# Kernel optimization log

Measured on AMD Instinct MI355X. Metric: run time of the kernel, lower is better.

Reference implementation:

```python
import jax, jax.numpy as jnp
import numpy as np

EMBED = 1024
HEADS = 16
HEAD_DIM = EMBED // HEADS


def setup_inputs() -> dict:
    key = jax.random.key(0)
    ks = jax.random.split(key, 8)
    N, S = 4, 2048
    inp = {
        "values": jax.random.normal(ks[0], (N, S, EMBED), jnp.float32),
        "keys": jax.random.normal(ks[1], (N, S, EMBED), jnp.float32),
        "queries": jax.random.normal(ks[2], (N, S, EMBED), jnp.float32),
        "mask": jnp.ones((N, S), jnp.int32),  # unused by the original forward
        # learned params (torch Linear: y = x @ W.T + b)
        "Wv": jax.random.normal(ks[3], (HEAD_DIM, HEAD_DIM), jnp.float32) / np.sqrt(HEAD_DIM),
        "Wk": jax.random.normal(ks[4], (HEAD_DIM, HEAD_DIM), jnp.float32) / np.sqrt(HEAD_DIM),
        "Wq": jax.random.normal(ks[5], (HEAD_DIM, HEAD_DIM), jnp.float32) / np.sqrt(HEAD_DIM),
        "Wo": jax.random.normal(ks[6], (EMBED, EMBED), jnp.float32) / np.sqrt(EMBED),
        "bo": jax.random.normal(ks[7], (EMBED,), jnp.float32) * 0.01,
    }
    return inp


def reference(values, keys, queries, mask, Wv, Wk, Wq, Wo, bo):
    N, S, _ = queries.shape
    # reshape to (N, len, heads, head_dim)
    v = values.reshape(N, S, HEADS, HEAD_DIM)
    k = keys.reshape(N, S, HEADS, HEAD_DIM)
    q = queries.reshape(N, S, HEADS, HEAD_DIM)
    # per-head linear projections (weights shared across heads), y = x @ W.T
    v = jnp.einsum('nlhd,ed->nlhe', v, Wv)
    k = jnp.einsum('nlhd,ed->nlhe', k, Wk)
    q = jnp.einsum('nlhd,ed->nlhe', q, Wq)
    # attention scores scaled by sqrt(embed_size), faithful to original
    scores = jnp.einsum('nqhd,nkhd->nhqk', q, k) / jnp.sqrt(jnp.float32(EMBED))
    attn = jax.nn.softmax(scores, axis=3)
    out = jnp.einsum('nhql,nlhd->nqhd', attn, v).reshape(N, S, EMBED)
    return out @ Wo.T + bo
```

## Files before the change

kernel.cpp:

```cpp
#include <hip/hip_runtime.h>


using f32x4  = __attribute__((ext_vector_type(4))) float;
using f32x16 = __attribute__((ext_vector_type(16))) float;
using bf16x8 = __attribute__((ext_vector_type(8))) __bf16;
using u32x4  = __attribute__((ext_vector_type(4))) unsigned int;
using u16x8  = __attribute__((ext_vector_type(8))) unsigned short;
typedef unsigned short u16;
typedef unsigned int   u32;
typedef unsigned long long u64;

#define SEQ 2048
#define EMB 1024
#define NHEADS 16
#define HDIM 64
#define NBATCH 4
#define NH 64

__device__ __forceinline__ u16 f2bf(float f) {
  u32 u = __builtin_bit_cast(u32, f);
  return (u16)((u + 0x7fffu + ((u >> 16) & 1u)) >> 16);
}

__device__ __forceinline__ u32 cvtpk_bf16(float a, float b) {
  u32 d;
  asm("v_cvt_pk_bf16_f32 %0, %1, %2" : "=v"(d) : "v"(a), "v"(b));
  return d;
}

__device__ __forceinline__ f32x4 mfma16(bf16x8 a, bf16x8 b, f32x4 c) {
  return __builtin_amdgcn_mfma_f32_16x16x32_bf16(a, b, c, 0, 0, 0);
}

__device__ __forceinline__ f32x16 mfma32(bf16x8 a, bf16x8 b, f32x16 c) {
  return __builtin_amdgcn_mfma_f32_32x32x16_bf16(a, b, c, 0, 0, 0);
}

__device__ __forceinline__ bf16x8 cvt8(f32x4 a, f32x4 b) {
  u32x4 r;
  r[0] = cvtpk_bf16(a[0], a[1]);
  r[1] = cvtpk_bf16(a[2], a[3]);
  r[2] = cvtpk_bf16(b[0], b[1]);
  r[3] = cvtpk_bf16(b[2], b[3]);
  return __builtin_bit_cast(bf16x8, r);
}

__device__ __forceinline__ float fexp2(float x) {
#if __has_builtin(__builtin_amdgcn_exp2f)
  return __builtin_amdgcn_exp2f(x);
#else
  return __expf(x * 0.6931471805599453f);
#endif
}

__device__ __forceinline__ void swap_words(u32 a, u32 b, int hi, u32& wlo, u32& whi) {
#if __has_builtin(__builtin_amdgcn_permlane32_swap)
  (void)hi;
  auto rr = __builtin_amdgcn_permlane32_swap((int)a, (int)b, false, false);
  wlo = (u32)rr[0];
  whi = (u32)rr[1];
#else
  u32 pa = (u32)__shfl_xor((int)a, 32);
  u32 pb = (u32)__shfl_xor((int)b, 32);
  wlo = hi ? pb : a;
  whi = hi ? b : pa;
#endif
}

__global__ __launch_bounds__(256) void proj_kernel(
    const float* __restrict__ Xq, const float* __restrict__ Xk, const float* __restrict__ Xv,
    const float* __restrict__ Wq, const float* __restrict__ Wk, const float* __restrict__ Wv,
    u16* __restrict__ Qp, u16* __restrict__ Kp, u16* __restrict__ Vp)
{
  int which = blockIdx.y;
  const float* X = which == 0 ? Xq : (which == 1 ? Xk : Xv);
  const float* W = which == 0 ? Wq : (which == 1 ? Wk : Wv);
  u16* Out = which == 0 ? Qp : (which == 1 ? Kp : Vp);
  float wscale = which == 0 ? 0.045084220027780106f : 1.0f;

  int t = threadIdx.x;
  int w = t >> 6, l = t & 63, l15 = l & 15, grp = l >> 4;
  int g0 = blockIdx.x * 64;

  bf16x8 wf[4][2];
#pragma unroll
  for (int nt = 0; nt < 4; nt++) {
    int c = nt * 16 + l15;
#pragma unroll
    for (int dc = 0; dc < 2; dc++) {
      const float* p = W + c * 64 + dc * 32 + grp * 8;
      f32x4 a = *(const f32x4*)p;
      f32x4 b = *(const f32x4*)(p + 4);
      a *= wscale; b *= wscale;
      wf[nt][dc] = cvt8(a, b);
    }
  }
  int grow = g0 + w * 16 + l15;
  const float* xr = X + (long)grow * 64;
  bf16x8 af[2];
#pragma unroll
  for (int dc = 0; dc < 2; dc++) {
    f32x4 a = *(const f32x4*)(xr + dc * 32 + grp * 8);
    f32x4 b = *(const f32x4*)(xr + dc * 32 + grp * 8 + 4);
    af[dc] = cvt8(a, b);
  }
  f32x4 acc[4] = {};
#pragma unroll
  for (int dc = 0; dc < 2; dc++)
#pragma unroll
    for (int nt = 0; nt < 4; nt++)
      acc[nt] = mfma16(af[dc], wf[nt][dc], acc[nt]);

#pragma unroll
  for (int r = 0; r < 4; r++) {
    int g = g0 + w * 16 + grp * 4 + r;
    int n = g >> 15;
    int s = (g >> 4) & 2047;
    int h = g & 15;
    u16* orow = Out + (((long)(n * NHEADS + h) * SEQ + s) << 6);
#pragma unroll
    for (int nt = 0; nt < 4; nt++)
      orow[nt * 16 + l15] = f2bf(acc[nt][r]);
  }
}

__global__ __launch_bounds__(256) void transpose_v(
    const u16* __restrict__ Vp, u16* __restrict__ Vt)
{
  int st = blockIdx.x;
  int nh = blockIdx.y;
  __shared__ u16 Vs[64 * 65];
  int t = threadIdx.x;
  const u16* src = Vp + ((long)nh * SEQ + st * 64) * 64;
#pragma unroll
  for (int p = 0; p < 2; p++) {
    int row = p * 32 + (t >> 3);
    int c0 = (t & 7) * 8;
    u32x4 u = *(const u32x4*)(src + row * 64 + c0);
    u16x8 v = __builtin_bit_cast(u16x8, u);
#pragma unroll
    for (int j = 0; j < 8; j++) Vs[(c0 + j) * 65 + row] = v[j];
  }
  __syncthreads();
  int e = t >> 2, k0 = (t & 3) * 16;
  u16x8 lo, hi;
#pragma unroll
  for (int j = 0; j < 8; j++) { lo[j] = Vs[e * 65 + k0 + j]; hi[j] = Vs[e * 65 + k0 + 8 + j]; }
  u16* dst = Vt + ((long)nh * 64 + e) * SEQ + st * 64 + k0;
  *(u32x4*)dst = __builtin_bit_cast(u32x4, lo);
  *(u32x4*)(dst + 8) = __builtin_bit_cast(u32x4, hi);
}

__global__ __launch_bounds__(256) void conv_wo(
    const float* __restrict__ Wo, u16* __restrict__ Wob)
{
  int i = (blockIdx.x * 256 + threadIdx.x) * 4;
  f32x4 v = *(const f32x4*)(Wo + i);
  u32 w0 = cvtpk_bf16(v[0], v[1]);
  u32 w1 = cvtpk_bf16(v[2], v[3]);
  u64 pk = (u64)w0 | ((u64)w1 << 32);
  *(u64*)(Wob + i) = pk;
}

__global__ __launch_bounds__(256, 3) void attn_kernel(
    const u16* __restrict__ Qp, const u16* __restrict__ Kp, const u16* __restrict__ Vt,
    u16* __restrict__ AO)
{
  int nh = blockIdx.x;
  int qb = blockIdx.y;
  int n = nh >> 4, h = nh & 15;

  __shared__ __align__(16) char smem[32768];

  int t = threadIdx.x, w = t >> 6, l = t & 63;
  int l31 = l & 31, hi = l >> 5;

  long qrow = (long)nh * SEQ + qb * 128 + w * 32 + l31;
  const char* qbase = (const char*)Qp + qrow * 128;
  bf16x8 qf[4];
#pragma unroll
  for (int dc = 0; dc < 4; dc++)
    qf[dc] = __builtin_bit_cast(bf16x8, *(const u32x4*)(qbase + dc * 32 + hi * 16));

  f32x16 o0 = {}, o1 = {};
  float mrun = -1e30f, lrun = 0.f;

  const char* Kg = (const char*)(Kp + (long)nh * SEQ * 64);
  const char* Vg = (const char*)(Vt + (long)nh * 64 * SEQ);

  int sr0 = t >> 3, sc = t & 7;
  int sr1 = sr0 + 32;
  int sphys0 = sr0 * 128 + ((sc ^ (sr0 & 7)) << 4);
  int sphys1 = sr1 * 128 + ((sc ^ (sr1 & 7)) << 4);

  u32x4 kreg[2], vreg[2];
  kreg[0] = *(const u32x4*)(Kg + sr0 * 128 + sc * 16);
  kreg[1] = *(const u32x4*)(Kg + sr1 * 128 + sc * 16);
  vreg[0] = *(const u32x4*)(Vg + (long)sr0 * 4096 + sc * 16);
  vreg[1] = *(const u32x4*)(Vg + (long)sr1 * 4096 + sc * 16);
  *(u32x4*)(smem + sphys0) = kreg[0];
  *(u32x4*)(smem + sphys1) = kreg[1];
  *(u32x4*)(smem + 8192 + sphys0) = vreg[0];
  *(u32x4*)(smem + 8192 + sphys1) = vreg[1];
  kreg[0] = *(const u32x4*)(Kg + 8192 + sr0 * 128 + sc * 16);
  kreg[1] = *(const u32x4*)(Kg + 8192 + sr1 * 128 + sc * 16);
  vreg[0] = *(const u32x4*)(Vg + (long)sr0 * 4096 + 128 + sc * 16);
  vreg[1] = *(const u32x4*)(Vg + (long)sr1 * 4096 + 128 + sc * 16);
  __syncthreads();

  for (int kt = 0; kt < 32; kt++) {
    const char* cur = smem + ((kt & 1) << 14);
    char* nxt = smem + (((kt + 1) & 1) << 14);
    const char* KsB = cur;
    const char* VsB = cur + 8192;

    f32x16 s0 = {}, s1 = {};
    __builtin_amdgcn_s_setprio(1);
#pragma unroll
    for (int dc = 0; dc < 4; dc++) {
      int cc = dc * 2 + hi;
      bf16x8 kf0 = __builtin_bit_cast(bf16x8,
          *(const u32x4*)(KsB + l31 * 128 + ((cc ^ (l31 & 7)) << 4)));
      s0 = mfma32(kf0, qf[dc], s0);
      int r1 = 32 + l31;
      bf16x8 kf1 = __builtin_bit_cast(bf16x8,
          *(const u32x4*)(KsB + r1 * 128 + ((cc ^ (r1 & 7)) << 4)));
      s1 = mfma32(kf1, qf[dc], s1);
    }
    __builtin_amdgcn_s_setprio(0);

    if (kt + 1 < 32) {
      *(u32x4*)(nxt + sphys0) = kreg[0];
      *(u32x4*)(nxt + sphys1) = kreg[1];
      *(u32x4*)(nxt + 8192 + sphys0) = vreg[0];
      *(u32x4*)(nxt + 8192 + sphys1) = vreg[1];
      if (kt + 2 < 32) {
        const char* Kt = Kg + (long)(kt + 2) * 8192;
        kreg[0] = *(const u32x4*)(Kt + sr0 * 128 + sc * 16);
        kreg[1] = *(const u32x4*)(Kt + sr1 * 128 + sc * 16);
        vreg[0] = *(const u32x4*)(Vg + (long)sr0 * 4096 + (kt + 2) * 128 + sc * 16);
        vreg[1] = *(const u32x4*)(Vg + (long)sr1 * 4096 + (kt + 2) * 128 + sc * 16);
      }
    }

    float m0 = fmaxf(s0[0], s1[0]), m1 = fmaxf(s0[1], s1[1]);
    float m2 = fmaxf(s0[2], s1[2]), m3 = fmaxf(s0[3], s1[3]);
#pragma unroll
    for (int r = 4; r < 16; r += 4) {
      m0 = fmaxf(m0, fmaxf(s0[r], s1[r]));
      m1 = fmaxf(m1, fmaxf(s0[r + 1], s1[r + 1]));
      m2 = fmaxf(m2, fmaxf(s0[r + 2], s1[r + 2]));
      m3 = fmaxf(m3, fmaxf(s0[r + 3], s1[r + 3]));
    }
    float mx = fmaxf(fmaxf(m0, m1), fmaxf(m2, m3));
    mx = fmaxf(mx, __shfl_xor(mx, 32));

    if (__any(mx > mrun + 8.0f)) {
      float mnew = fmaxf(mrun, mx);
      float scl = fexp2(mrun - mnew);
      mrun = mnew;
      lrun *= scl;
#pragma unroll
      for (int r = 0; r < 16; r++) { o0[r] *= scl; o1[r] *= scl; }
    }
#pragma unroll
    for (int r = 0; r < 16; r++) s0[r] = fexp2(s0[r] - mrun);
#pragma unroll
    for (int r = 0; r < 16; r++) s1[r] = fexp2(s1[r] - mrun);

    {
      f32x16 sv = s0 + s1;
      f32x4 q4 = { sv[0] + sv[4], sv[1] + sv[5], sv[2] + sv[6], sv[3] + sv[7] };
      f32x4 q5 = { sv[8] + sv[12], sv[9] + sv[13], sv[10] + sv[14], sv[11] + sv[15] };
      f32x4 q6 = q4 + q5;
      lrun += (q6[0] + q6[1]) + (q6[2] + q6[3]);
    }

    bf16x8 pB[4];
    {
      u32 xw[8], wq[16];
#pragma unroll
      for (int i = 0; i < 8; i++) xw[i] = cvtpk_bf16(s0[2 * i], s0[2 * i + 1]);
      swap_words(xw[0], xw[2], hi, wq[0], wq[2]);
      swap_words(xw[1], xw[3], hi, wq[1], wq[3]);
      swap_words(xw[4], xw[6], hi, wq[4], wq[6]);
      swap_words(xw[5], xw[7], hi, wq[5], wq[7]);
#pragma unroll
      for (int i = 0; i < 8; i++) xw[i] = cvtpk_bf16(s1[2 * i], s1[2 * i + 1]);
      swap_words(xw[0], xw[2], hi, wq[8], wq[10]);
      swap_words(xw[1], xw[3], hi, wq[9], wq[11]);
      swap_words(xw[4], xw[6], hi, wq[12], wq[14]);
      swap_words(xw[5], xw[7], hi, wq[13], wq[15]);
#pragma unroll
      for (int kb = 0; kb < 4; kb++) {
        u32x4 v4 = { wq[kb * 4 + 0], wq[kb * 4 + 1], wq[kb * 4 + 2], wq[kb * 4 + 3] };
        pB[kb] = __builtin_bit_cast(bf16x8, v4);
      }
    }

    __builtin_amdgcn_s_setprio(1);
#pragma unroll
    for (int kb = 0; kb < 4; kb++) {
      int cc = kb * 2 + hi;
      bf16x8 vf0 = __builtin_bit_cast(bf16x8,
          *(const u32x4*)(VsB + l31 * 128 + ((cc ^ (l31 & 7)) << 4)));
      o0 = mfma32(vf0, pB[kb], o0);
      int r1 = 32 + l31;
      bf16x8 vf1 = __builtin_bit_cast(bf16x8,
          *(const u32x4*)(VsB + r1 * 128 + ((cc ^ (r1 & 7)) << 4)));
      o1 = mfma32(vf1, pB[kb], o1);
    }
    __builtin_amdgcn_s_setprio(0);

    __syncthreads();
  }

  lrun += __shfl_xor(lrun, 32);
  float inv = 1.0f / lrun;
  int qlocal = w * 32 + l31;
  char* OsmB = smem;
#pragma unroll
  for (int i = 0; i < 8; i++) {
    int e0 = ((2 * i) & 3) + 8 * ((2 * i) >> 2) + 4 * hi;
    u32 pk0 = cvtpk_bf16(o0[2 * i] * inv, o0[2 * i + 1] * inv);
    *(u32*)(OsmB + qlocal * 144 + 2 * e0) = pk0;
    u32 pk1 = cvtpk_bf16(o1[2 * i] * inv, o1[2 * i + 1] * inv);
    *(u32*)(OsmB + qlocal * 144 + 2 * (e0 + 32)) = pk1;
  }
  __syncthreads();
  int qr = t >> 1, half = t & 1;
  const char* src = OsmB + qr * 144 + half * 64;
  long qg = (long)qb * 128 + qr;
  char* dst = (char*)(AO + ((long)n * SEQ + qg) * EMB + h * 64 + half * 32);
#pragma unroll
  for (int j = 0; j < 4; j++)
    *(u32x4*)(dst + j * 16) = *(const u32x4*)(src + j * 16);
}

__global__ __launch_bounds__(256) void gemm_out(
    const u16* __restrict__ A, const u16* __restrict__ B,
    const float* __restrict__ bias, float* __restrict__ C)
{
  int bm = blockIdx.x, bn = blockIdx.y;
  __shared__ __align__(16) char gsm[32768];
  int t = threadIdx.x, w = t >> 6, l = t & 63, l15 = l & 15, grp = l >> 4;
  int wm = w >> 1, wn = w & 1;
  f32x4 acc[4][4] = {};
  const char* Ab = (const char*)(A + (long)bm * 128 * 1024);
  const char* Bb = (const char*)(B + (long)bn * 128 * 1024);

  int srow = t >> 2, sc2 = t & 3;
  int srow1 = srow + 64;
  int sp0 = srow * 64 + ((sc2 ^ ((srow >> 1) & 3)) << 4);
  int sp1 = srow1 * 64 + ((sc2 ^ ((srow1 >> 1) & 3)) << 4);

  u32x4 areg[2], breg[2];
  areg[0] = *(const u32x4*)(Ab + (long)srow * 2048 + sc2 * 16);
  areg[1] = *(const u32x4*)(Ab + (long)srow1 * 2048 + sc2 * 16);
  breg[0] = *(const u32x4*)(Bb + (long)srow * 2048 + sc2 * 16);
  breg[1] = *(const u32x4*)(Bb + (long)srow1 * 2048 + sc2 * 16);
  *(u32x4*)(gsm + sp0) = areg[0];
  *(u32x4*)(gsm + sp1) = areg[1];
  *(u32x4*)(gsm + 8192 + sp0) = breg[0];
  *(u32x4*)(gsm + 8192 + sp1) = breg[1];
  areg[0] = *(const u32x4*)(Ab + (long)srow * 2048 + 64 + sc2 * 16);
  areg[1] = *(const u32x4*)(Ab + (long)srow1 * 2048 + 64 + sc2 * 16);
  breg[0] = *(const u32x4*)(Bb + (long)srow * 2048 + 64 + sc2 * 16);
  breg[1] = *(const u32x4*)(Bb + (long)srow1 * 2048 + 64 + sc2 * 16);
  __syncthreads();

  for (int kt = 0; kt < 32; kt++) {
    const char* AsB = gsm + ((kt & 1) << 14);
    const char* BsB = AsB + 8192;
    char* nxt = gsm + (((kt + 1) & 1) << 14);

    bf16x8 af[4], bf_[4];
#pragma unroll
    for (int i = 0; i < 4; i++) {
      int row = wm * 64 + i * 16 + l15;
      af[i] = __builtin_bit_cast(bf16x8,
          *(const u32x4*)(AsB + row * 64 + ((grp ^ ((row >> 1) & 3)) << 4)));
      int rowb = wn * 64 + i * 16 + l15;
      bf_[i] = __builtin_bit_cast(bf16x8,
          *(const u32x4*)(BsB + rowb * 64 + ((grp ^ ((rowb >> 1) & 3)) << 4)));
    }

    if (kt + 1 < 32) {
      *(u32x4*)(nxt + sp0) = areg[0];
      *(u32x4*)(nxt + sp1) = areg[1];
      *(u32x4*)(nxt + 8192 + sp0) = breg[0];
      *(u32x4*)(nxt + 8192 + sp1) = breg[1];
      if (kt + 2 < 32) {
        areg[0] = *(const u32x4*)(Ab + (long)srow * 2048 + (kt + 2) * 64 + sc2 * 16);
        areg[1] = *(const u32x4*)(Ab + (long)srow1 * 2048 + (kt + 2) * 64 + sc2 * 16);
        breg[0] = *(const u32x4*)(Bb + (long)srow * 2048 + (kt + 2) * 64 + sc2 * 16);
        breg[1] = *(const u32x4*)(Bb + (long)srow1 * 2048 + (kt + 2) * 64 + sc2 * 16);
      }
    }

    __builtin_amdgcn_s_setprio(1);
#pragma unroll
    for (int i = 0; i < 4; i++)
#pragma unroll
      for (int j = 0; j < 4; j++)
        acc[i][j] = mfma16(af[i], bf_[j], acc[i][j]);
    __builtin_amdgcn_s_setprio(0);

    __syncthreads();
  }

  float bv[4];
#pragma unroll
  for (int j = 0; j < 4; j++) bv[j] = bias[bn * 128 + wn * 64 + j * 16 + l15];
#pragma unroll
  for (int i = 0; i < 4; i++) {
#pragma unroll
    for (int r = 0; r < 4; r++) {
      long row = (long)bm * 128 + wm * 64 + i * 16 + grp * 4 + r;
      float* crow = C + row * 1024 + bn * 128 + wn * 64;
#pragma unroll
      for (int j = 0; j < 4; j++)
        crow[j * 16 + l15] = acc[i][j][r] + bv[j];
    }
  }
}

extern "C" void kernel_launch(void* const* d_in, const int* in_sizes, int n_in,
                              void* d_out, int out_size, void* d_ws, size_t ws_size,
                              hipStream_t stream)
{
  const float* Vx = (const float*)d_in[0];
  const float* Kx = (const float*)d_in[1];
  const float* Qx = (const float*)d_in[2];
  const float* Wv = (const float*)d_in[4];
  const float* Wk = (const float*)d_in[5];
  const float* Wq = (const float*)d_in[6];
  const float* Wo = (const float*)d_in[7];
  const float* bo = (const float*)d_in[8];
  float* out = (float*)d_out;
  char* ws = (char*)d_ws;

  u16* Qp  = (u16*)(ws);
  u16* Kp  = (u16*)(ws + (1L << 24));
  u16* Vt  = (u16*)(ws + (2L << 24));
  u16* Vp  = (u16*)(ws + (3L << 24));
  u16* AO  = Vp;
  u16* Wob = (u16*)(ws + (4L << 24));

  proj_kernel<<<dim3(2048, 3), 256, 0, stream>>>(Qx, Kx, Vx, Wq, Wk, Wv, Qp, Kp, Vp);
  transpose_v<<<dim3(32, 64), 256, 0, stream>>>(Vp, Vt);
  conv_wo<<<1024, 256, 0, stream>>>(Wo, Wob);
  attn_kernel<<<dim3(64, 16), 256, 0, stream>>>(Qp, Kp, Vt, AO);
  gemm_out<<<dim3(64, 8), 256, 0, stream>>>(AO, Wob, bo, out);
}
```

Baseline: 190.0 us.

## Process two query tiles per wave in attention to reuse K/V fragments

Result: slower. 268.5 us (+41.4%).

```diff
diff --git a/kernel.cpp b/kernel.cpp
--- a/kernel.cpp
+++ b/kernel.cpp
@@ -162,7 +162,97 @@
   *(u64*)(Wob + i) = pk;
 }
 
-__global__ __launch_bounds__(256, 3) void attn_kernel(
+
+#define LDV(off) __builtin_bit_cast(bf16x8, *(const u32x4*)(smem + (off)))
+
+#define SM_PACK(s0, s1, mrun, lrun, o0, o1, pB) do {                       \
+    f32x16 _sv;                                                            \
+    _Pragma("unroll")                                                      \
+    for (int r = 0; r < 16; r++) _sv[r] = fmaxf(s0[r], s1[r]);             \
+    float _a0 = fmaxf(fmaxf(_sv[0], _sv[1]), fmaxf(_sv[2], _sv[3]));       \
+    float _a1 = fmaxf(fmaxf(_sv[4], _sv[5]), fmaxf(_sv[6], _sv[7]));       \
+    float _a2 = fmaxf(fmaxf(_sv[8], _sv[9]), fmaxf(_sv[10], _sv[11]));     \
+    float _a3 = fmaxf(fmaxf(_sv[12], _sv[13]), fmaxf(_sv[14], _sv[15]));   \
+    float _mx = fmaxf(fmaxf(_a0, _a1), fmaxf(_a2, _a3));                   \
+    _mx = fmaxf(_mx, __shfl_xor(_mx, 32));                                 \
+    if (__any(_mx > (mrun) + 8.0f)) {                                      \
+      float _mn = fmaxf((mrun), _mx);                                      \
+      float _scl = fexp2((mrun) - _mn);                                    \
+      (mrun) = _mn; (lrun) *= _scl;                                        \
+      _Pragma("unroll")                                                    \
+      for (int r = 0; r < 16; r++) { (o0)[r] *= _scl; (o1)[r] *= _scl; }   \
+    }                                                                      \
+    _Pragma("unroll")                                                      \
+    for (int r = 0; r < 16; r++) s0[r] = fexp2(s0[r] - (mrun));            \
+    _Pragma("unroll")                                                      \
+    for (int r = 0; r < 16; r++) s1[r] = fexp2(s1[r] - (mrun));            \
+    { f32x16 _ss = s0 + s1;                                                \
+      f32x4 _q4 = { _ss[0]+_ss[4], _ss[1]+_ss[5], _ss[2]+_ss[6], _ss[3]+_ss[7] };      \
+      f32x4 _q5 = { _ss[8]+_ss[12], _ss[9]+_ss[13], _ss[10]+_ss[14], _ss[11]+_ss[15] };\
+      f32x4 _q6 = _q4 + _q5;                                               \
+      (lrun) += (_q6[0] + _q6[1]) + (_q6[2] + _q6[3]); }                   \
+    { u32 _xw[8], _wq[16];                                                 \
+      _Pragma("unroll")                                                    \
+      for (int i = 0; i < 8; i++) _xw[i] = cvtpk_bf16(s0[2*i], s0[2*i+1]); \
+      swap_words(_xw[0], _xw[2], hi, _wq[0], _wq[2]);                      \
+      swap_words(_xw[1], _xw[3], hi, _wq[1], _wq[3]);                      \
+      swap_words(_xw[4], _xw[6], hi, _wq[4], _wq[6]);                      \
+      swap_words(_xw[5], _xw[7], hi, _wq[5], _wq[7]);                      \
+      _Pragma("unroll")                                                    \
+      for (int i = 0; i < 8; i++) _xw[i] = cvtpk_bf16(s1[2*i], s1[2*i+1]); \
+      swap_words(_xw[0], _xw[2], hi, _wq[8], _wq[10]);                     \
+      swap_words(_xw[1], _xw[3], hi, _wq[9], _wq[11]);                     \
+      swap_words(_xw[4], _xw[6], hi, _wq[12], _wq[14]);                    \
+      swap_words(_xw[5], _xw[7], hi, _wq[13], _wq[15]);                    \
+      _Pragma("unroll")                                                    \
+      for (int kb = 0; kb < 4; kb++) {                                     \
+        u32x4 _v4 = { _wq[kb*4+0], _wq[kb*4+1], _wq[kb*4+2], _wq[kb*4+3] };\
+        (pB)[kb] = __builtin_bit_cast(bf16x8, _v4); } }                    \
+  } while (0)
+
+#define ATTN_STEP(CUROFF, DOSTAGE, DOPREF) do {                            \
+    f32x16 sA0 = {}, sA1 = {}, sB0 = {}, sB1 = {};                         \
+    __builtin_amdgcn_s_setprio(1);                                         \
+    _Pragma("unroll")                                                      \
+    for (int dc = 0; dc < 4; dc++) {                                       \
+      bf16x8 kf0 = LDV(koff[dc*2+0] + (CUROFF));                           \
+      bf16x8 kf1 = LDV(koff[dc*2+1] + (CUROFF));                           \
+      sA0 = mfma32(kf0, qfA[dc], sA0);                                     \
+      sB0 = mfma32(kf0, qfB[dc], sB0);                                     \
+      sA1 = mfma32(kf1, qfA[dc], sA1);                                     \
+      sB1 = mfma32(kf1, qfB[dc], sB1);                                     \
+    }                                                                      \
+    __builtin_amdgcn_s_setprio(0);                                         \
+    if (DOSTAGE) {                                                         \
+      *(u32x4*)(smem + sphys0 + ((CUROFF) ^ 16384)) = kreg[0];             \
+      *(u32x4*)(smem + sphys1 + ((CUROFF) ^ 16384)) = kreg[1];             \
+      *(u32x4*)(smem + sphys0 + 8192 + ((CUROFF) ^ 16384)) = vreg[0];      \
+      *(u32x4*)(smem + sphys1 + 8192 + ((CUROFF) ^ 16384)) = vreg[1];      \
+      if (DOPREF) {                                                        \
+        kreg[0] = *(const u32x4*)kp0; kp0 += 8192;                         \
+        kreg[1] = *(const u32x4*)kp1; kp1 += 8192;                         \
+        vreg[0] = *(const u32x4*)vp0; vp0 += 128;                          \
+        vreg[1] = *(const u32x4*)vp1; vp1 += 128;                          \
+      }                                                                    \
+    }                                                                      \
+    bf16x8 pBA[4], pBB[4];                                                 \
+    SM_PACK(sA0, sA1, mA, lA, oA0, oA1, pBA);                              \
+    SM_PACK(sB0, sB1, mB, lB, oB0, oB1, pBB);                              \
+    __builtin_amdgcn_s_setprio(1);                                         \
+    _Pragma("unroll")                                                      \
+    for (int kb = 0; kb < 4; kb++) {                                       \
+      bf16x8 vf0 = LDV(koff[kb*2+0] + 8192 + (CUROFF));                    \
+      bf16x8 vf1 = LDV(koff[kb*2+1] + 8192 + (CUROFF));                    \
+      oA0 = mfma32(vf0, pBA[kb], oA0);                                     \
+      oB0 = mfma32(vf0, pBB[kb], oB0);                                     \
+      oA1 = mfma32(vf1, pBA[kb], oA1);                                     \
+      oB1 = mfma32(vf1, pBB[kb], oB1);                                     \
+    }                                                                      \
+    __builtin_amdgcn_s_setprio(0);                                         \
+    __syncthreads();                                                       \
+  } while (0)
+
+__global__ __launch_bounds__(256, 2) void attn_kernel(
     const u16* __restrict__ Qp, const u16* __restrict__ Kp, const u16* __restrict__ Vt,
     u16* __restrict__ AO)
 {
@@ -170,170 +260,81 @@
   int qb = blockIdx.y;
   int n = nh >> 4, h = nh & 15;
 
-  __shared__ __align__(16) char smem[32768];
+  __shared__ __align__(16) char smem[36864];
 
   int t = threadIdx.x, w = t >> 6, l = t & 63;
   int l31 = l & 31, hi = l >> 5;
 
-  long qrow = (long)nh * SEQ + qb * 128 + w * 32 + l31;
-  const char* qbase = (const char*)Qp + qrow * 128;
-  bf16x8 qf[4];
+  long qrow0 = (long)nh * SEQ + qb * 256 + w * 64 + l31;
+  const char* qbase0 = (const char*)Qp + qrow0 * 128;
+  bf16x8 qfA[4], qfB[4];
+#pragma unroll
+  for (int dc = 0; dc < 4; dc++) {
+    qfA[dc] = __builtin_bit_cast(bf16x8, *(const u32x4*)(qbase0 + dc * 32 + hi * 16));
+    qfB[dc] = __builtin_bit_cast(bf16x8, *(const u32x4*)(qbase0 + 32 * 128 + dc * 32 + hi * 16));
+  }
+
+  f32x16 oA0 = {}, oA1 = {}, oB0 = {}, oB1 = {};
+  float mA = -1e30f, lA = 0.f, mB = -1e30f, lB = 0.f;
+
+  int koff[8];
 #pragma unroll
   for (int dc = 0; dc < 4; dc++)
-    qf[dc] = __builtin_bit_cast(bf16x8, *(const u32x4*)(qbase + dc * 32 + hi * 16));
-
-  f32x16 o0 = {}, o1 = {};
-  float mrun = -1e30f, lrun = 0.f;
+#pragma unroll
+    for (int half = 0; half < 2; half++) {
+      int row = half * 32 + l31;
+      int cc = dc * 2 + hi;
+      koff[dc * 2 + half] = row * 128 + ((cc ^ (row & 7)) << 4);
+    }
+
+  int sr0 = t >> 3, sc = t & 7, sr1 = sr0 + 32;
+  int sphys0 = sr0 * 128 + ((sc ^ (sr0 & 7)) << 4);
+  int sphys1 = sr1 * 128 + ((sc ^ (sr1 & 7)) << 4);
 
   const char* Kg = (const char*)(Kp + (long)nh * SEQ * 64);
   const char* Vg = (const char*)(Vt + (long)nh * 64 * SEQ);
-
-  int sr0 = t >> 3, sc = t & 7;
-  int sr1 = sr0 + 32;
-  int sphys0 = sr0 * 128 + ((sc ^ (sr0 & 7)) << 4);
-  int sphys1 = sr1 * 128 + ((sc ^ (sr1 & 7)) << 4);
+  const char* kp0 = Kg + sr0 * 128 + sc * 16;
+  const char* kp1 = Kg + sr1 * 128 + sc * 16;
+  const char* vp0 = Vg + (long)sr0 * 4096 + sc * 16;
+  const char* vp1 = Vg + (long)sr1 * 4096 + sc * 16;
 
   u32x4 kreg[2], vreg[2];
-  kreg[0] = *(const u32x4*)(Kg + sr0 * 128 + sc * 16);
-  kreg[1] = *(const u32x4*)(Kg + sr1 * 128 + sc * 16);
-  vreg[0] = *(const u32x4*)(Vg + (long)sr0 * 4096 + sc * 16);
-  vreg[1] = *(const u32x4*)(Vg + (long)sr1 * 4096 + sc * 16);
+  kreg[0] = *(const u32x4*)kp0;
+  kreg[1] = *(const u32x4*)kp1;
+  vreg[0] = *(const u32x4*)vp0;
+  vreg[1] = *(const u32x4*)vp1;
   *(u32x4*)(smem + sphys0) = kreg[0];
   *(u32x4*)(smem + sphys1) = kreg[1];
   *(u32x4*)(smem + 8192 + sphys0) = vreg[0];
   *(u32x4*)(smem + 8192 + sphys1) = vreg[1];
-  kreg[0] = *(const u32x4*)(Kg + 8192 + sr0 * 128 + sc * 16);
-  kreg[1] = *(const u32x4*)(Kg + 8192 + sr1 * 128 + sc * 16);
-  vreg[0] = *(const u32x4*)(Vg + (long)sr0 * 4096 + 128 + sc * 16);
-  vreg[1] = *(const u32x4*)(Vg + (long)sr1 * 4096 + 128 + sc * 16);
+  kreg[0] = *(const u32x4*)(kp0 + 8192); kp0 += 16384;
+  kreg[1] = *(const u32x4*)(kp1 + 8192); kp1 += 16384;
+  vreg[0] = *(const u32x4*)(vp0 + 128);  vp0 += 256;
+  vreg[1] = *(const u32x4*)(vp1 + 128);  vp1 += 256;
   __syncthreads();
 
-  for (int kt = 0; kt < 32; kt++) {
-    const char* cur = smem + ((kt & 1) << 14);
-    char* nxt = smem + (((kt + 1) & 1) << 14);
-    const char* KsB = cur;
-    const char* VsB = cur + 8192;
-
-    f32x16 s0 = {}, s1 = {};
-    __builtin_amdgcn_s_setprio(1);
-#pragma unroll
-    for (int dc = 0; dc < 4; dc++) {
-      int cc = dc * 2 + hi;
-      bf16x8 kf0 = __builtin_bit_cast(bf16x8,
-          *(const u32x4*)(KsB + l31 * 128 + ((cc ^ (l31 & 7)) << 4)));
-      s0 = mfma32(kf0, qf[dc], s0);
-      int r1 = 32 + l31;
-      bf16x8 kf1 = __builtin_bit_cast(bf16x8,
-          *(const u32x4*)(KsB + r1 * 128 + ((cc ^ (r1 & 7)) << 4)));
-      s1 = mfma32(kf1, qf[dc], s1);
-    }
-    __builtin_amdgcn_s_setprio(0);
-
-    if (kt + 1 < 32) {
-      *(u32x4*)(nxt + sphys0) = kreg[0];
-      *(u32x4*)(nxt + sphys1) = kreg[1];
-      *(u32x4*)(nxt + 8192 + sphys0) = vreg[0];
-      *(u32x4*)(nxt + 8192 + sphys1) = vreg[1];
-      if (kt + 2 < 32) {
-        const char* Kt = Kg + (long)(kt + 2) * 8192;
-        kreg[0] = *(const u32x4*)(Kt + sr0 * 128 + sc * 16);
-        kreg[1] = *(const u32x4*)(Kt + sr1 * 128 + sc * 16);
-        vreg[0] = *(const u32x4*)(Vg + (long)sr0 * 4096 + (kt + 2) * 128 + sc * 16);
-        vreg[1] = *(const u32x4*)(Vg + (long)sr1 * 4096 + (kt + 2) * 128 + sc * 16);
-      }
-    }
-
-    float m0 = fmaxf(s0[0], s1[0]), m1 = fmaxf(s0[1], s1[1]);
-    float m2 = fmaxf(s0[2], s1[2]), m3 = fmaxf(s0[3], s1[3]);
-#pragma unroll
-    for (int r = 4; r < 16; r += 4) {
-      m0 = fmaxf(m0, fmaxf(s0[r], s1[r]));
-      m1 = fmaxf(m1, fmaxf(s0[r + 1], s1[r + 1]));
-      m2 = fmaxf(m2, fmaxf(s0[r + 2], s1[r + 2]));
-      m3 = fmaxf(m3, fmaxf(s0[r + 3], s1[r + 3]));
-    }
-    float mx = fmaxf(fmaxf(m0, m1), fmaxf(m2, m3));
-    mx = fmaxf(mx, __shfl_xor(mx, 32));
-
-    if (__any(mx > mrun + 8.0f)) {
-      float mnew = fmaxf(mrun, mx);
-      float scl = fexp2(mrun - mnew);
-      mrun = mnew;
-      lrun *= scl;
-#pragma unroll
-      for (int r = 0; r < 16; r++) { o0[r] *= scl; o1[r] *= scl; }
-    }
-#pragma unroll
-    for (int r = 0; r < 16; r++) s0[r] = fexp2(s0[r] - mrun);
-#pragma unroll
-    for (int r = 0; r < 16; r++) s1[r] = fexp2(s1[r] - mrun);
-
-    {
-      f32x16 sv = s0 + s1;
-      f32x4 q4 = { sv[0] + sv[4], sv[1] + sv[5], sv[2] + sv[6], sv[3] + sv[7] };
-      f32x4 q5 = { sv[8] + sv[12], sv[9] + sv[13], sv[10] + sv[14], sv[11] + sv[15] };
-      f32x4 q6 = q4 + q5;
-      lrun += (q6[0] + q6[1]) + (q6[2] + q6[3]);
-    }
-
-    bf16x8 pB[4];
-    {
-      u32 xw[8], wq[16];
-#pragma unroll
-      for (int i = 0; i < 8; i++) xw[i] = cvtpk_bf16(s0[2 * i], s0[2 * i + 1]);
-      swap_words(xw[0], xw[2], hi, wq[0], wq[2]);
-      swap_words(xw[1], xw[3], hi, wq[1], wq[3]);
-      swap_words(xw[4], xw[6], hi, wq[4], wq[6]);
-      swap_words(xw[5], xw[7], hi, wq[5], wq[7]);
-#pragma unroll
-      for (int i = 0; i < 8; i++) xw[i] = cvtpk_bf16(s1[2 * i], s1[2 * i + 1]);
-      swap_words(xw[0], xw[2], hi, wq[8], wq[10]);
-      swap_words(xw[1], xw[3], hi, wq[9], wq[11]);
-      swap_words(xw[4], xw[6], hi, wq[12], wq[14]);
-      swap_words(xw[5], xw[7], hi, wq[13], wq[15]);
-#pragma unroll
-      for (int kb = 0; kb < 4; kb++) {
-        u32x4 v4 = { wq[kb * 4 + 0], wq[kb * 4 + 1], wq[kb * 4 + 2], wq[kb * 4 + 3] };
-        pB[kb] = __builtin_bit_cast(bf16x8, v4);
-      }
-    }
-
-    __builtin_amdgcn_s_setprio(1);
-#pragma unroll
-    for (int kb = 0; kb < 4; kb++) {
-      int cc = kb * 2 + hi;
-      bf16x8 vf0 = __builtin_bit_cast(bf16x8,
-          *(const u32x4*)(VsB + l31 * 128 + ((cc ^ (l31 & 7)) << 4)));
-      o0 = mfma32(vf0, pB[kb], o0);
-      int r1 = 32 + l31;
-      bf16x8 vf1 = __builtin_bit_cast(bf16x8,
-          *(const u32x4*)(VsB + r1 * 128 + ((cc ^ (r1 & 7)) << 4)));
-      o1 = mfma32(vf1, pB[kb], o1);
-    }
-    __builtin_amdgcn_s_setprio(0);
-
-    __syncthreads();
-  }
-
-  lrun += __shfl_xor(lrun, 32);
-  float inv = 1.0f / lrun;
-  int qlocal = w * 32 + l31;
-  char* OsmB = smem;
+  for (int kt2 = 0; kt2 < 16; kt2++) {
+    ATTN_STEP(0, true, (kt2 < 15));
+    ATTN_STEP(16384, (kt2 < 15), (kt2 < 15));
+  }
+
+  lA += __shfl_xor(lA, 32);
+  lB += __shfl_xor(lB, 32);
+  float invA = 1.0f / lA, invB = 1.0f / lB;
+  int qlA = w * 64 + l31;
 #pragma unroll
   for (int i = 0; i < 8; i++) {
     int e0 = ((2 * i) & 3) + 8 * ((2 * i) >> 2) + 4 * hi;
-    u32 pk0 = cvtpk_bf16(o0[2 * i] * inv, o0[2 * i + 1] * inv);
-    *(u32*)(OsmB + qlocal * 144 + 2 * e0) = pk0;
-    u32 pk1 = cvtpk_bf16(o1[2 * i] * inv, o1[2 * i + 1] * inv);
-    *(u32*)(OsmB + qlocal * 144 + 2 * (e0 + 32)) = pk1;
+    *(u32*)(smem + qlA * 144 + 2 * e0) = cvtpk_bf16(oA0[2*i] * invA, oA0[2*i+1] * invA);
+    *(u32*)(smem + qlA * 144 + 2 * (e0 + 32)) = cvtpk_bf16(oA1[2*i] * invA, oA1[2*i+1] * invA);
+    *(u32*)(smem + (qlA + 32) * 144 + 2 * e0) = cvtpk_bf16(oB0[2*i] * invB, oB0[2*i+1] * invB);
+    *(u32*)(smem + (qlA + 32) * 144 + 2 * (e0 + 32)) = cvtpk_bf16(oB1[2*i] * invB, oB1[2*i+1] * invB);
   }
   __syncthreads();
-  int qr = t >> 1, half = t & 1;
-  const char* src = OsmB + qr * 144 + half * 64;
-  long qg = (long)qb * 128 + qr;
-  char* dst = (char*)(AO + ((long)n * SEQ + qg) * EMB + h * 64 + half * 32);
-#pragma unroll
-  for (int j = 0; j < 4; j++)
+  const char* src = smem + t * 144;
+  char* dst = (char*)(AO + ((long)n * SEQ + qb * 256 + t) * EMB + h * 64);
+#pragma unroll
+  for (int j = 0; j < 8; j++)
     *(u32x4*)(dst + j * 16) = *(const u32x4*)(src + j * 16);
 }
 
@@ -450,6 +451,6 @@
   proj_kernel<<<dim3(2048, 3), 256, 0, stream>>>(Qx, Kx, Vx, Wq, Wk, Wv, Qp, Kp, Vp);
   transpose_v<<<dim3(32, 64), 256, 0, stream>>>(Vp, Vt);
   conv_wo<<<1024, 256, 0, stream>>>(Wo, Wob);
-  attn_kernel<<<dim3(64, 16), 256, 0, stream>>>(Qp, Kp, Vt, AO);
+  attn_kernel<<<dim3(64, 8), 256, 0, stream>>>(Qp, Kp, Vt, AO);
   gemm_out<<<dim3(64, 8), 256, 0, stream>>>(AO, Wob, bo, out);
 }
```
